# Kernel tuning notes

Hardware: AMD Instinct MI355X
Metric: run time of the kernel (lower is better)

The kernel has to match this reference:

```python
import jax, jax.numpy as jnp
import numpy as np

N_NODES = 100000
N_EDGES = 1600000
N_GRAPHS = 512
IN_DIM = 128
HID = 128
N_CLASSES = 10


def _gcn_conv(x, W, b, src, dst, n):
    """PyG GCNConv: out = D^{-1/2} (A+I) D^{-1/2} (x @ W) + b."""
    xw = x @ W  # [n, out_dim]
    loop = jnp.arange(n)
    s = jnp.concatenate([src, loop])  # add self loops
    d = jnp.concatenate([dst, loop])
    deg = jax.ops.segment_sum(jnp.ones(s.shape, dtype=xw.dtype), d, num_segments=n)
    dinv = jnp.where(deg > 0, jax.lax.rsqrt(deg), jnp.zeros((), xw.dtype))
    norm = dinv[s] * dinv[d]  # [E + n]
    out = jax.ops.segment_sum(xw[s] * norm[:, None], d, num_segments=n)
    return out + b


def _global_mean_pool(x, batch, num_graphs):
    sums = jax.ops.segment_sum(x, batch, num_segments=num_graphs)
    cnts = jax.ops.segment_sum(jnp.ones(batch.shape, dtype=x.dtype), batch, num_segments=num_graphs)
    return sums / jnp.maximum(cnts, 1.0)[:, None]


def setup_inputs() -> dict:
    key = jax.random.key(0)
    ks = jax.random.split(key, 8)
    x = jax.random.normal(ks[0], (N_NODES, IN_DIM), dtype=jnp.float32)
    edge_index = jax.random.randint(ks[1], (2, N_EDGES), 0, N_NODES, dtype=jnp.int64)
    batch = jnp.sort(jax.random.randint(ks[2], (N_NODES,), 0, N_GRAPHS, dtype=jnp.int64))
    sc = 1.0 / np.sqrt(IN_DIM)
    W1 = jax.random.normal(ks[3], (IN_DIM, HID), dtype=jnp.float32) * sc
    b1 = jnp.zeros((HID,), dtype=jnp.float32)
    W2 = jax.random.normal(ks[4], (HID, HID), dtype=jnp.float32) * (1.0 / np.sqrt(HID))
    b2 = jnp.zeros((HID,), dtype=jnp.float32)
    Wc = jax.random.normal(ks[5], (HID, N_CLASSES), dtype=jnp.float32) * (1.0 / np.sqrt(HID))
    bc = jnp.zeros((N_CLASSES,), dtype=jnp.float32)
    return {"x": x, "edge_index": edge_index, "batch": batch,
            "W1": W1, "b1": b1, "W2": W2, "b2": b2, "Wc": Wc, "bc": bc}


def reference(x, edge_index, batch, W1, b1, W2, b2, Wc, bc):
    src, dst = edge_index[0], edge_index[1]
    n = x.shape[0]
    h = _gcn_conv(x, W1, b1, src, dst, n)
    h = jax.nn.relu(h)
    h = _gcn_conv(h, W2, b2, src, dst, n)
    g = _global_mean_pool(h, batch, N_GRAPHS)
    return g @ Wc + bc
```

## Files before the change

kernel.cpp:

```cpp
#include <hip/hip_runtime.h>

#define N_NODES 100000
#define N_EDGES 1600000
#define N_GRAPHS 512
#define DIM 128
#define NCLS 10
#define NBKT 782
#define BCAP 2560

typedef __attribute__((ext_vector_type(8))) short short8;
typedef __attribute__((ext_vector_type(4))) float f32x4;

static __device__ __forceinline__ unsigned short f2bf(float f) {
    unsigned u = __float_as_uint(f);
    unsigned r = (u + 0x7FFF + ((u >> 16) & 1)) >> 16;
    return (unsigned short)r;
}
static __device__ __forceinline__ float bf2f(unsigned u) {
    return __uint_as_float(u << 16);
}


__global__ __launch_bounds__(256) void k_bucket(
    const int* __restrict__ src, const int* __restrict__ dst,
    int* __restrict__ bcnt, unsigned* __restrict__ bpack, int E) {
    __shared__ int cnt[NBKT];
    __shared__ int base[NBKT];
    int tid = threadIdx.x;
    for (int i = tid; i < NBKT; i += 256) cnt[i] = 0;
    __syncthreads();
    int e0 = blockIdx.x * 4096 + tid;
    unsigned pk[16]; short bk[16];
#pragma unroll
    for (int j = 0; j < 16; j++) {
        int e = e0 + j * 256;
        if (e < E) {
            int s = src[e], d = dst[e];
            bk[j] = (short)(d >> 7);
            pk[j] = ((unsigned)(d & 127) << 17) | (unsigned)s;
            atomicAdd(&cnt[bk[j]], 1);
        } else bk[j] = -1;
    }
    __syncthreads();
    for (int i = tid; i < NBKT; i += 256) {
        int c = cnt[i];
        base[i] = c ? atomicAdd(&bcnt[i], c) : 0;
        cnt[i] = 0;
    }
    __syncthreads();
#pragma unroll
    for (int j = 0; j < 16; j++) {
        if (bk[j] >= 0) {
            int p = base[bk[j]] + atomicAdd(&cnt[bk[j]], 1);
            if (p < BCAP) bpack[(size_t)bk[j] * BCAP + p] = pk[j];
        }
    }
}

__global__ __launch_bounds__(256) void k_bscan(const int* __restrict__ bcnt,
                                               int* __restrict__ bbase) {
    __shared__ int lds[256];
    int tid = threadIdx.x;
    int v[4], pre[4];
    int s = 0;
#pragma unroll
    for (int j = 0; j < 4; j++) {
        int idx = tid * 4 + j;
        v[j] = (idx < NBKT) ? min(bcnt[idx], BCAP) : 0;
        pre[j] = s; s += v[j];
    }
    lds[tid] = s;
    __syncthreads();
    for (int off = 1; off < 256; off <<= 1) {
        int t = (tid >= off) ? lds[tid - off] : 0;
        __syncthreads();
        lds[tid] += t;
        __syncthreads();
    }
    int excl = lds[tid] - s;
#pragma unroll
    for (int j = 0; j < 4; j++) {
        int idx = tid * 4 + j;
        if (idx < NBKT) bbase[idx] = excl + pre[j];
    }
}

__global__ __launch_bounds__(256) void k_bsort(
    const unsigned* __restrict__ bpack, const int* __restrict__ bcnt,
    const int* __restrict__ bbase, int* __restrict__ rp, float* __restrict__ dinv,
    int* __restrict__ esrc, int N) {
    __shared__ int cnt[128];
    __shared__ int scan[128];
    __shared__ int cur[128];
    int b = blockIdx.x, tid = threadIdx.x;
    int n0 = b << 7;
    int m = min(bcnt[b], BCAP);
    int gbase = bbase[b];
    const unsigned* bp = bpack + (size_t)b * BCAP;
    if (tid < 128) cnt[tid] = 0;
    __syncthreads();
    for (int j = tid; j < m; j += 256) atomicAdd(&cnt[bp[j] >> 17], 1);
    __syncthreads();
    if (tid < 128) scan[tid] = cnt[tid];
    __syncthreads();
    for (int off = 1; off < 128; off <<= 1) {
        int t = (tid < 128 && tid >= off) ? scan[tid - off] : 0;
        __syncthreads();
        if (tid < 128) scan[tid] += t;
        __syncthreads();
    }
    if (tid < 128) {
        int c = cnt[tid];
        int excl = scan[tid] - c;
        int node = n0 + tid;
        if (node <= N) rp[node] = gbase + excl;
        if (node < N) dinv[node] = rsqrtf((float)(c + 1));
        cur[tid] = gbase + excl;
    }
    __syncthreads();
    for (int j = tid; j < m; j += 256) {
        unsigned pk = bp[j];
        int p = atomicAdd(&cur[pk >> 17], 1);
        esrc[p] = (int)(pk & 0x1FFFF);
    }
}


__global__ void k_wprep(const float* __restrict__ W1, const float* __restrict__ W2,
                        unsigned short* __restrict__ wf1, unsigned short* __restrict__ wf2) {
    int b = blockIdx.x;
    const float* W = (b < 64) ? W1 : W2;
    unsigned short* wfrag = (b < 64) ? wf1 : wf2;
    int t = (b & 63) * 256 + threadIdx.x;
    int j = t & 7, lane = (t >> 3) & 63, nt = (t >> 9) & 7, kit = t >> 12;
    int k = kit * 32 + (lane >> 4) * 8 + j;
    int n = nt * 16 + (lane & 15);
    float v = W[k * 128 + n];
    unsigned short h = f2bf(v);
    wfrag[t] = h;
    wfrag[16384 + t] = f2bf(v - bf2f(h));
}


__global__ __launch_bounds__(256) void k_gemm_f32(
    const float* __restrict__ A, const unsigned short* __restrict__ wfrag,
    const float* __restrict__ dinv, unsigned short* __restrict__ ybf, int M) {
    __shared__ unsigned short scr[4 * 32 * 136];
    int tid = threadIdx.x, wave = tid >> 6, lane = tid & 63;
    int m = lane & 15, quad = lane >> 4;
    int rowBase = blockIdx.x * 128 + wave * 32;
    int r0 = rowBase + m, r1 = rowBase + 16 + m;
    f32x4 acc0[8], acc1[8];
#pragma unroll
    for (int i = 0; i < 8; i++) { acc0[i] = (f32x4){0,0,0,0}; acc1[i] = (f32x4){0,0,0,0}; }
    const unsigned short* whi = wfrag;
    const unsigned short* wlo = wfrag + 16384;

#pragma unroll
    for (int kit = 0; kit < 4; kit++) {
        float a0[8], a1[8];
        if (r0 < M) {
            const float4* ap = (const float4*)(A + (size_t)r0 * 128 + kit * 32 + quad * 8);
            float4 f0 = ap[0], f1 = ap[1];
            a0[0]=f0.x; a0[1]=f0.y; a0[2]=f0.z; a0[3]=f0.w; a0[4]=f1.x; a0[5]=f1.y; a0[6]=f1.z; a0[7]=f1.w;
        } else { for (int j = 0; j < 8; j++) a0[j] = 0.f; }
        if (r1 < M) {
            const float4* ap = (const float4*)(A + (size_t)r1 * 128 + kit * 32 + quad * 8);
            float4 f0 = ap[0], f1 = ap[1];
            a1[0]=f0.x; a1[1]=f0.y; a1[2]=f0.z; a1[3]=f0.w; a1[4]=f1.x; a1[5]=f1.y; a1[6]=f1.z; a1[7]=f1.w;
        } else { for (int j = 0; j < 8; j++) a1[j] = 0.f; }
        short8 ahi0, alo0, ahi1, alo1;
#pragma unroll
        for (int j = 0; j < 8; j++) {
            unsigned short h0 = f2bf(a0[j]);
            ahi0[j] = (short)h0; alo0[j] = (short)f2bf(a0[j] - bf2f(h0));
            unsigned short h1 = f2bf(a1[j]);
            ahi1[j] = (short)h1; alo1[j] = (short)f2bf(a1[j] - bf2f(h1));
        }
        int fb = kit * 4096 + lane * 8;
#pragma unroll
        for (int nt = 0; nt < 8; nt++) {
            int idx = fb + nt * 512;
            short8 bhi = *(const short8*)(whi + idx);
            short8 blo = *(const short8*)(wlo + idx);
            acc0[nt] = __builtin_amdgcn_mfma_f32_16x16x32_bf16(ahi0, bhi, acc0[nt], 0, 0, 0);
            acc0[nt] = __builtin_amdgcn_mfma_f32_16x16x32_bf16(alo0, bhi, acc0[nt], 0, 0, 0);
            acc0[nt] = __builtin_amdgcn_mfma_f32_16x16x32_bf16(ahi0, blo, acc0[nt], 0, 0, 0);
            acc1[nt] = __builtin_amdgcn_mfma_f32_16x16x32_bf16(ahi1, bhi, acc1[nt], 0, 0, 0);
            acc1[nt] = __builtin_amdgcn_mfma_f32_16x16x32_bf16(alo1, bhi, acc1[nt], 0, 0, 0);
            acc1[nt] = __builtin_amdgcn_mfma_f32_16x16x32_bf16(ahi1, blo, acc1[nt], 0, 0, 0);
        }
    }
    float dv0 = (r0 < M) ? dinv[r0] : 0.f;
    float dv1 = (r1 < M) ? dinv[r1] : 0.f;
    unsigned short* wsm = scr + wave * 32 * 136;
#pragma unroll
    for (int rg = 0; rg < 4; rg++) {
        float s0 = __shfl(dv0, quad * 4 + rg);
        float s1 = __shfl(dv1, quad * 4 + rg);
#pragma unroll
        for (int nt = 0; nt < 8; nt++) {
            wsm[(quad * 4 + rg) * 136 + nt * 16 + m] = f2bf(acc0[nt][rg] * s0);
            wsm[(16 + quad * 4 + rg) * 136 + nt * 16 + m] = f2bf(acc1[nt][rg] * s1);
        }
    }
    __syncthreads();
#pragma unroll
    for (int i = 0; i < 8; i++) {
        int rl = i * 4 + quad;
        int grow = rowBase + rl;
        if (grow < M) {
            short8 v = *(const short8*)(wsm + rl * 136 + m * 8);
            *(short8*)(ybf + (size_t)grow * 128 + m * 8) = v;
        }
    }
}


__global__ __launch_bounds__(256) void k_gemm_bf(
    const unsigned short* __restrict__ A, const unsigned short* __restrict__ wfrag,
    const float* __restrict__ dinv, unsigned short* __restrict__ ybf, int M) {
    __shared__ unsigned short scr[4 * 32 * 136];
    int tid = threadIdx.x, wave = tid >> 6, lane = tid & 63;
    int m = lane & 15, quad = lane >> 4;
    int rowBase = blockIdx.x * 128 + wave * 32;
    int r0 = rowBase + m, r1 = rowBase + 16 + m;
    f32x4 acc0[8], acc1[8];
#pragma unroll
    for (int i = 0; i < 8; i++) { acc0[i] = (f32x4){0,0,0,0}; acc1[i] = (f32x4){0,0,0,0}; }
    const unsigned short* whi = wfrag;
    const unsigned short* wlo = wfrag + 16384;

#pragma unroll
    for (int kit = 0; kit < 4; kit++) {
        short8 ah0, ah1;
        if (r0 < M) ah0 = *(const short8*)(A + (size_t)r0 * 128 + kit * 32 + quad * 8);
        else { for (int j = 0; j < 8; j++) ah0[j] = 0; }
        if (r1 < M) ah1 = *(const short8*)(A + (size_t)r1 * 128 + kit * 32 + quad * 8);
        else { for (int j = 0; j < 8; j++) ah1[j] = 0; }
        int fb = kit * 4096 + lane * 8;
#pragma unroll
        for (int nt = 0; nt < 8; nt++) {
            int idx = fb + nt * 512;
            short8 bhi = *(const short8*)(whi + idx);
            short8 blo = *(const short8*)(wlo + idx);
            acc0[nt] = __builtin_amdgcn_mfma_f32_16x16x32_bf16(ah0, bhi, acc0[nt], 0, 0, 0);
            acc0[nt] = __builtin_amdgcn_mfma_f32_16x16x32_bf16(ah0, blo, acc0[nt], 0, 0, 0);
            acc1[nt] = __builtin_amdgcn_mfma_f32_16x16x32_bf16(ah1, bhi, acc1[nt], 0, 0, 0);
            acc1[nt] = __builtin_amdgcn_mfma_f32_16x16x32_bf16(ah1, blo, acc1[nt], 0, 0, 0);
        }
    }
    float dv0 = (r0 < M) ? dinv[r0] : 0.f;
    float dv1 = (r1 < M) ? dinv[r1] : 0.f;
    unsigned short* wsm = scr + wave * 32 * 136;
#pragma unroll
    for (int rg = 0; rg < 4; rg++) {
        float s0 = __shfl(dv0, quad * 4 + rg);
        float s1 = __shfl(dv1, quad * 4 + rg);
#pragma unroll
        for (int nt = 0; nt < 8; nt++) {
            wsm[(quad * 4 + rg) * 136 + nt * 16 + m] = f2bf(acc0[nt][rg] * s0);
            wsm[(16 + quad * 4 + rg) * 136 + nt * 16 + m] = f2bf(acc1[nt][rg] * s1);
        }
    }
    __syncthreads();
#pragma unroll
    for (int i = 0; i < 8; i++) {
        int rl = i * 4 + quad;
        int grow = rowBase + rl;
        if (grow < M) {
            short8 v = *(const short8*)(wsm + rl * 136 + m * 8);
            *(short8*)(ybf + (size_t)grow * 128 + m * 8) = v;
        }
    }
}


__global__ __launch_bounds__(256) void k_agg(
    const unsigned short* __restrict__ y, const float* __restrict__ dinv,
    const int* __restrict__ rp, const int* __restrict__ esrc,
    const float* __restrict__ bias, unsigned* __restrict__ out, int relu, int N) {
    int wave = threadIdx.x >> 6;
    int lane = threadIdx.x & 63;
    int node = blockIdx.x * 4 + wave;
    if (node >= N) return;
    const unsigned* y2 = (const unsigned*)y;
    unsigned vs = y2[(size_t)node * 64 + lane];
    float a0 = bf2f(vs & 0xFFFF), a1 = bf2f(vs >> 16);
    int beg = rp[node], end = rp[node + 1];
    int j = beg;
    for (; j + 8 <= end; j += 8) {
        int s0 = esrc[j], s1 = esrc[j + 1], s2 = esrc[j + 2], s3 = esrc[j + 3];
        int s4 = esrc[j + 4], s5 = esrc[j + 5], s6 = esrc[j + 6], s7 = esrc[j + 7];
        unsigned v0 = y2[(size_t)s0 * 64 + lane];
        unsigned v1 = y2[(size_t)s1 * 64 + lane];
        unsigned v2 = y2[(size_t)s2 * 64 + lane];
        unsigned v3 = y2[(size_t)s3 * 64 + lane];
        unsigned v4 = y2[(size_t)s4 * 64 + lane];
        unsigned v5 = y2[(size_t)s5 * 64 + lane];
        unsigned v6 = y2[(size_t)s6 * 64 + lane];
        unsigned v7 = y2[(size_t)s7 * 64 + lane];
        a0 += bf2f(v0 & 0xFFFF); a1 += bf2f(v0 >> 16);
        a0 += bf2f(v1 & 0xFFFF); a1 += bf2f(v1 >> 16);
        a0 += bf2f(v2 & 0xFFFF); a1 += bf2f(v2 >> 16);
        a0 += bf2f(v3 & 0xFFFF); a1 += bf2f(v3 >> 16);
        a0 += bf2f(v4 & 0xFFFF); a1 += bf2f(v4 >> 16);
        a0 += bf2f(v5 & 0xFFFF); a1 += bf2f(v5 >> 16);
        a0 += bf2f(v6 & 0xFFFF); a1 += bf2f(v6 >> 16);
        a0 += bf2f(v7 & 0xFFFF); a1 += bf2f(v7 >> 16);
    }
    for (; j < end; j++) {
        unsigned v = y2[(size_t)esrc[j] * 64 + lane];
        a0 += bf2f(v & 0xFFFF); a1 += bf2f(v >> 16);
    }
    float s = dinv[node];
    float2 bv = ((const float2*)bias)[lane];
    float o0 = s * a0 + bv.x;
    float o1 = s * a1 + bv.y;
    if (relu) { o0 = fmaxf(o0, 0.f); o1 = fmaxf(o1, 0.f); }
    out[(size_t)node * 64 + lane] = (unsigned)f2bf(o0) | ((unsigned)f2bf(o1) << 16);
}


__global__ __launch_bounds__(256) void k_poolhead(
    const unsigned* __restrict__ h2, const int* __restrict__ batch,
    const float* __restrict__ Wc, const float* __restrict__ bc,
    float* __restrict__ out, int n) {
    __shared__ float2 red[4][64];
    __shared__ float grow[DIM];
    int gid = blockIdx.x;
    int tid = threadIdx.x, wave = tid >> 6, lane = tid & 63;
    int lo = 0, hi = n;
    while (lo < hi) { int mid = (lo + hi) >> 1; if (batch[mid] < gid) lo = mid + 1; else hi = mid; }
    int start = lo;
    hi = n;
    while (lo < hi) { int mid = (lo + hi) >> 1; if (batch[mid] < gid + 1) lo = mid + 1; else hi = mid; }
    int end = lo;
    float a0 = 0.f, a1 = 0.f;
    for (int r = start + wave; r < end; r += 4) {
        unsigned v = h2[(size_t)r * 64 + lane];
        a0 += bf2f(v & 0xFFFF); a1 += bf2f(v >> 16);
    }
    red[wave][lane] = make_float2(a0, a1);
    __syncthreads();
    if (tid < 64) {
        float2 s = red[0][tid];
        s.x += red[1][tid].x; s.y += red[1][tid].y;
        s.x += red[2][tid].x; s.y += red[2][tid].y;
        s.x += red[3][tid].x; s.y += red[3][tid].y;
        int cnt = end - start;
        float inv = 1.f / (float)(cnt > 0 ? cnt : 1);
        grow[tid * 2] = s.x * inv;
        grow[tid * 2 + 1] = s.y * inv;
    }
    __syncthreads();
    if (tid < NCLS) {
        float acc = bc[tid];
#pragma unroll 16
        for (int k = 0; k < DIM; k++) acc += grow[k] * Wc[k * NCLS + tid];
        out[gid * NCLS + tid] = acc;
    }
}

extern "C" void kernel_launch(void* const* d_in, const int* in_sizes, int n_in,
                              void* d_out, int out_size, void* d_ws, size_t ws_size,
                              hipStream_t stream) {
    const float* x    = (const float*)d_in[0];
    const int*   ei   = (const int*)d_in[1];
    const int*   batch= (const int*)d_in[2];
    const float* W1   = (const float*)d_in[3];
    const float* b1   = (const float*)d_in[4];
    const float* W2   = (const float*)d_in[5];
    const float* b2   = (const float*)d_in[6];
    const float* Wc   = (const float*)d_in[7];
    const float* bc   = (const float*)d_in[8];
    float* out = (float*)d_out;
    const int N = N_NODES, E = N_EDGES;
    const int* src = ei;
    const int* dst = ei + E;

    char* ws = (char*)d_ws;
    size_t off = 0;
    auto carve = [&](size_t bytes) -> void* {
        void* p = ws + off;
        off = (off + bytes + 255) & ~(size_t)255;
        return p;
    };
    int*      rp    = (int*)     carve((size_t)(N + 1) * 4);
    float*    dinv  = (float*)   carve((size_t)N * 4);
    int*      bcnt  = (int*)     carve(NBKT * 4);
    int*      bbase = (int*)     carve(NBKT * 4);
    unsigned* bpack = (unsigned*)carve((size_t)NBKT * BCAP * 4);
    int*      esrc  = (int*)     carve((size_t)E * 4);
    unsigned short* wf1 = (unsigned short*)carve(2 * 16384 * 2);
    unsigned short* wf2 = (unsigned short*)carve(2 * 16384 * 2);
    unsigned short* bufY = (unsigned short*)carve((size_t)N * DIM * 2);
    unsigned short* bufH = (unsigned short*)carve((size_t)N * DIM * 2);
    (void)ws_size; (void)n_in; (void)in_sizes; (void)out_size;

    hipMemsetAsync(bcnt, 0, NBKT * 4, stream);
    hipLaunchKernelGGL(k_wprep,  dim3(128), dim3(256), 0, stream, W1, W2, wf1, wf2);
    hipLaunchKernelGGL(k_bucket, dim3((E + 4095) / 4096), dim3(256), 0, stream, src, dst, bcnt, bpack, E);
    hipLaunchKernelGGL(k_bscan,  dim3(1), dim3(256), 0, stream, bcnt, bbase);
    hipLaunchKernelGGL(k_bsort,  dim3(NBKT), dim3(256), 0, stream, bpack, bcnt, bbase, rp, dinv, esrc, N);

    int gemmGrid = (N + 127) / 128;
    hipLaunchKernelGGL(k_gemm_f32, dim3(gemmGrid), dim3(256), 0, stream, x, wf1, dinv, bufY, N);
    hipLaunchKernelGGL(k_agg, dim3((N + 3) / 4), dim3(256), 0, stream, bufY, dinv, rp, esrc, b1, (unsigned*)bufH, 1, N);
    hipLaunchKernelGGL(k_gemm_bf, dim3(gemmGrid), dim3(256), 0, stream, bufH, wf2, dinv, bufY, N);
    hipLaunchKernelGGL(k_agg, dim3((N + 3) / 4), dim3(256), 0, stream, bufY, dinv, rp, esrc, b2, (unsigned*)bufH, 0, N);
    hipLaunchKernelGGL(k_poolhead, dim3(N_GRAPHS), dim3(256), 0, stream, (const unsigned*)bufH, batch, Wc, bc, out, N);
}
```

Measured before the change: 375.3 us.

## Fold memset and bucket scan into other kernels, stage weights in LDS, wave-load edge indices

Zeroing the bucket counters moves into extra blocks of the weight-prep kernel, which drops the memset. The single-block bucket scan is now recomputed redundantly inside every bucket-sort block, which removes two launches. Both GEMM kernels copy the high-part weight fragments into shared memory and read them from there. The aggregation loop loads up to 64 edge indices per wave in one coalesced load and broadcasts them with shuffles instead of issuing scalar index loads.

```diff
diff --git a/kernel.cpp b/kernel.cpp
--- a/kernel.cpp
+++ b/kernel.cpp
@@ -21,114 +21,15 @@
 }
 
 
-__global__ __launch_bounds__(256) void k_bucket(
-    const int* __restrict__ src, const int* __restrict__ dst,
-    int* __restrict__ bcnt, unsigned* __restrict__ bpack, int E) {
-    __shared__ int cnt[NBKT];
-    __shared__ int base[NBKT];
-    int tid = threadIdx.x;
-    for (int i = tid; i < NBKT; i += 256) cnt[i] = 0;
-    __syncthreads();
-    int e0 = blockIdx.x * 4096 + tid;
-    unsigned pk[16]; short bk[16];
-#pragma unroll
-    for (int j = 0; j < 16; j++) {
-        int e = e0 + j * 256;
-        if (e < E) {
-            int s = src[e], d = dst[e];
-            bk[j] = (short)(d >> 7);
-            pk[j] = ((unsigned)(d & 127) << 17) | (unsigned)s;
-            atomicAdd(&cnt[bk[j]], 1);
-        } else bk[j] = -1;
-    }
-    __syncthreads();
-    for (int i = tid; i < NBKT; i += 256) {
-        int c = cnt[i];
-        base[i] = c ? atomicAdd(&bcnt[i], c) : 0;
-        cnt[i] = 0;
-    }
-    __syncthreads();
-#pragma unroll
-    for (int j = 0; j < 16; j++) {
-        if (bk[j] >= 0) {
-            int p = base[bk[j]] + atomicAdd(&cnt[bk[j]], 1);
-            if (p < BCAP) bpack[(size_t)bk[j] * BCAP + p] = pk[j];
-        }
-    }
-}
-
-__global__ __launch_bounds__(256) void k_bscan(const int* __restrict__ bcnt,
-                                               int* __restrict__ bbase) {
-    __shared__ int lds[256];
-    int tid = threadIdx.x;
-    int v[4], pre[4];
-    int s = 0;
-#pragma unroll
-    for (int j = 0; j < 4; j++) {
-        int idx = tid * 4 + j;
-        v[j] = (idx < NBKT) ? min(bcnt[idx], BCAP) : 0;
-        pre[j] = s; s += v[j];
-    }
-    lds[tid] = s;
-    __syncthreads();
-    for (int off = 1; off < 256; off <<= 1) {
-        int t = (tid >= off) ? lds[tid - off] : 0;
-        __syncthreads();
-        lds[tid] += t;
-        __syncthreads();
-    }
-    int excl = lds[tid] - s;
-#pragma unroll
-    for (int j = 0; j < 4; j++) {
-        int idx = tid * 4 + j;
-        if (idx < NBKT) bbase[idx] = excl + pre[j];
-    }
-}
-
-__global__ __launch_bounds__(256) void k_bsort(
-    const unsigned* __restrict__ bpack, const int* __restrict__ bcnt,
-    const int* __restrict__ bbase, int* __restrict__ rp, float* __restrict__ dinv,
-    int* __restrict__ esrc, int N) {
-    __shared__ int cnt[128];
-    __shared__ int scan[128];
-    __shared__ int cur[128];
-    int b = blockIdx.x, tid = threadIdx.x;
-    int n0 = b << 7;
-    int m = min(bcnt[b], BCAP);
-    int gbase = bbase[b];
-    const unsigned* bp = bpack + (size_t)b * BCAP;
-    if (tid < 128) cnt[tid] = 0;
-    __syncthreads();
-    for (int j = tid; j < m; j += 256) atomicAdd(&cnt[bp[j] >> 17], 1);
-    __syncthreads();
-    if (tid < 128) scan[tid] = cnt[tid];
-    __syncthreads();
-    for (int off = 1; off < 128; off <<= 1) {
-        int t = (tid < 128 && tid >= off) ? scan[tid - off] : 0;
-        __syncthreads();
-        if (tid < 128) scan[tid] += t;
-        __syncthreads();
-    }
-    if (tid < 128) {
-        int c = cnt[tid];
-        int excl = scan[tid] - c;
-        int node = n0 + tid;
-        if (node <= N) rp[node] = gbase + excl;
-        if (node < N) dinv[node] = rsqrtf((float)(c + 1));
-        cur[tid] = gbase + excl;
-    }
-    __syncthreads();
-    for (int j = tid; j < m; j += 256) {
-        unsigned pk = bp[j];
-        int p = atomicAdd(&cur[pk >> 17], 1);
-        esrc[p] = (int)(pk & 0x1FFFF);
-    }
-}
-
-
 __global__ void k_wprep(const float* __restrict__ W1, const float* __restrict__ W2,
-                        unsigned short* __restrict__ wf1, unsigned short* __restrict__ wf2) {
+                        unsigned short* __restrict__ wf1, unsigned short* __restrict__ wf2,
+                        int* __restrict__ bcnt) {
     int b = blockIdx.x;
+    if (b >= 128) {
+        int i = (b - 128) * 256 + threadIdx.x;
+        if (i < NBKT) bcnt[i] = 0;
+        return;
+    }
     const float* W = (b < 64) ? W1 : W2;
     unsigned short* wfrag = (b < 64) ? wf1 : wf2;
     int t = (b & 63) * 256 + threadIdx.x;
@@ -142,18 +43,117 @@
 }
 
 
+__global__ __launch_bounds__(256) void k_bucket(
+    const int* __restrict__ src, const int* __restrict__ dst,
+    int* __restrict__ bcnt, unsigned* __restrict__ bpack, int E) {
+    __shared__ int cnt[NBKT];
+    __shared__ int base[NBKT];
+    int tid = threadIdx.x;
+    for (int i = tid; i < NBKT; i += 256) cnt[i] = 0;
+    __syncthreads();
+    int e0 = blockIdx.x * 4096 + tid;
+    unsigned pk[16]; short bk[16];
+#pragma unroll
+    for (int j = 0; j < 16; j++) {
+        int e = e0 + j * 256;
+        if (e < E) {
+            int s = src[e], d = dst[e];
+            bk[j] = (short)(d >> 7);
+            pk[j] = ((unsigned)(d & 127) << 17) | (unsigned)s;
+            atomicAdd(&cnt[bk[j]], 1);
+        } else bk[j] = -1;
+    }
+    __syncthreads();
+    for (int i = tid; i < NBKT; i += 256) {
+        int c = cnt[i];
+        base[i] = c ? atomicAdd(&bcnt[i], c) : 0;
+        cnt[i] = 0;
+    }
+    __syncthreads();
+#pragma unroll
+    for (int j = 0; j < 16; j++) {
+        if (bk[j] >= 0) {
+            int p = base[bk[j]] + atomicAdd(&cnt[bk[j]], 1);
+            if (p < BCAP) bpack[(size_t)bk[j] * BCAP + p] = pk[j];
+        }
+    }
+}
+
+
+__global__ __launch_bounds__(256) void k_bsort(
+    const unsigned* __restrict__ bpack, const int* __restrict__ bcnt,
+    int* __restrict__ rp, float* __restrict__ dinv,
+    int* __restrict__ esrc, int N) {
+    __shared__ int lds[256];
+    __shared__ int gbase_sh;
+    __shared__ int cnt[128];
+    __shared__ int scan[128];
+    __shared__ int cur[128];
+    int b = blockIdx.x, tid = threadIdx.x;
+    int v[4], pre[4];
+    int s = 0;
+#pragma unroll
+    for (int j = 0; j < 4; j++) {
+        int idx = tid * 4 + j;
+        v[j] = (idx < NBKT) ? min(bcnt[idx], BCAP) : 0;
+        pre[j] = s; s += v[j];
+    }
+    lds[tid] = s;
+    __syncthreads();
+    for (int off = 1; off < 256; off <<= 1) {
+        int t = (tid >= off) ? lds[tid - off] : 0;
+        __syncthreads();
+        lds[tid] += t;
+        __syncthreads();
+    }
+    if (tid == (b >> 2)) gbase_sh = lds[tid] - s + pre[b & 3];
+    if (tid < 128) cnt[tid] = 0;
+    __syncthreads();
+    int gbase = gbase_sh;
+    int n0 = b << 7;
+    int m = min(bcnt[b], BCAP);
+    const unsigned* bp = bpack + (size_t)b * BCAP;
+    for (int j = tid; j < m; j += 256) atomicAdd(&cnt[bp[j] >> 17], 1);
+    __syncthreads();
+    if (tid < 128) scan[tid] = cnt[tid];
+    __syncthreads();
+    for (int off = 1; off < 128; off <<= 1) {
+        int t = (tid < 128 && tid >= off) ? scan[tid - off] : 0;
+        __syncthreads();
+        if (tid < 128) scan[tid] += t;
+        __syncthreads();
+    }
+    if (tid < 128) {
+        int c = cnt[tid];
+        int excl = scan[tid] - c;
+        int node = n0 + tid;
+        if (node <= N) rp[node] = gbase + excl;
+        if (node < N) dinv[node] = rsqrtf((float)(c + 1));
+        cur[tid] = gbase + excl;
+    }
+    __syncthreads();
+    for (int j = tid; j < m; j += 256) {
+        unsigned pk = bp[j];
+        int p = atomicAdd(&cur[pk >> 17], 1);
+        esrc[p] = (int)(pk & 0x1FFFF);
+    }
+}
+
+
 __global__ __launch_bounds__(256) void k_gemm_f32(
     const float* __restrict__ A, const unsigned short* __restrict__ wfrag,
     const float* __restrict__ dinv, unsigned short* __restrict__ ybf, int M) {
-    __shared__ unsigned short scr[4 * 32 * 136];
+    __shared__ unsigned short ldsw[4 * 32 * 136];
     int tid = threadIdx.x, wave = tid >> 6, lane = tid & 63;
     int m = lane & 15, quad = lane >> 4;
     int rowBase = blockIdx.x * 128 + wave * 32;
     int r0 = rowBase + m, r1 = rowBase + 16 + m;
+    for (int i = tid; i < 2048; i += 256)
+        ((short8*)ldsw)[i] = ((const short8*)wfrag)[i];
+    __syncthreads();
     f32x4 acc0[8], acc1[8];
 #pragma unroll
     for (int i = 0; i < 8; i++) { acc0[i] = (f32x4){0,0,0,0}; acc1[i] = (f32x4){0,0,0,0}; }
-    const unsigned short* whi = wfrag;
     const unsigned short* wlo = wfrag + 16384;
 
 #pragma unroll
@@ -181,7 +181,7 @@
 #pragma unroll
         for (int nt = 0; nt < 8; nt++) {
             int idx = fb + nt * 512;
-            short8 bhi = *(const short8*)(whi + idx);
+            short8 bhi = *(const short8*)(ldsw + idx);
             short8 blo = *(const short8*)(wlo + idx);
             acc0[nt] = __builtin_amdgcn_mfma_f32_16x16x32_bf16(ahi0, bhi, acc0[nt], 0, 0, 0);
             acc0[nt] = __builtin_amdgcn_mfma_f32_16x16x32_bf16(alo0, bhi, acc0[nt], 0, 0, 0);
@@ -191,9 +191,10 @@
             acc1[nt] = __builtin_amdgcn_mfma_f32_16x16x32_bf16(ahi1, blo, acc1[nt], 0, 0, 0);
         }
     }
+    __syncthreads();
     float dv0 = (r0 < M) ? dinv[r0] : 0.f;
     float dv1 = (r1 < M) ? dinv[r1] : 0.f;
-    unsigned short* wsm = scr + wave * 32 * 136;
+    unsigned short* wsm = ldsw + wave * 32 * 136;
 #pragma unroll
     for (int rg = 0; rg < 4; rg++) {
         float s0 = __shfl(dv0, quad * 4 + rg);
@@ -220,15 +221,17 @@
 __global__ __launch_bounds__(256) void k_gemm_bf(
     const unsigned short* __restrict__ A, const unsigned short* __restrict__ wfrag,
     const float* __restrict__ dinv, unsigned short* __restrict__ ybf, int M) {
-    __shared__ unsigned short scr[4 * 32 * 136];
+    __shared__ unsigned short ldsw[4 * 32 * 136];
     int tid = threadIdx.x, wave = tid >> 6, lane = tid & 63;
     int m = lane & 15, quad = lane >> 4;
     int rowBase = blockIdx.x * 128 + wave * 32;
     int r0 = rowBase + m, r1 = rowBase + 16 + m;
+    for (int i = tid; i < 2048; i += 256)
+        ((short8*)ldsw)[i] = ((const short8*)wfrag)[i];
+    __syncthreads();
     f32x4 acc0[8], acc1[8];
 #pragma unroll
     for (int i = 0; i < 8; i++) { acc0[i] = (f32x4){0,0,0,0}; acc1[i] = (f32x4){0,0,0,0}; }
-    const unsigned short* whi = wfrag;
     const unsigned short* wlo = wfrag + 16384;
 
 #pragma unroll
@@ -242,7 +245,7 @@
 #pragma unroll
         for (int nt = 0; nt < 8; nt++) {
             int idx = fb + nt * 512;
-            short8 bhi = *(const short8*)(whi + idx);
+            short8 bhi = *(const short8*)(ldsw + idx);
             short8 blo = *(const short8*)(wlo + idx);
             acc0[nt] = __builtin_amdgcn_mfma_f32_16x16x32_bf16(ah0, bhi, acc0[nt], 0, 0, 0);
             acc0[nt] = __builtin_amdgcn_mfma_f32_16x16x32_bf16(ah0, blo, acc0[nt], 0, 0, 0);
@@ -250,9 +253,10 @@
             acc1[nt] = __builtin_amdgcn_mfma_f32_16x16x32_bf16(ah1, blo, acc1[nt], 0, 0, 0);
         }
     }
+    __syncthreads();
     float dv0 = (r0 < M) ? dinv[r0] : 0.f;
     float dv1 = (r1 < M) ? dinv[r1] : 0.f;
-    unsigned short* wsm = scr + wave * 32 * 136;
+    unsigned short* wsm = ldsw + wave * 32 * 136;
 #pragma unroll
     for (int rg = 0; rg < 4; rg++) {
         float s0 = __shfl(dv0, quad * 4 + rg);
@@ -289,29 +293,30 @@
     float a0 = bf2f(vs & 0xFFFF), a1 = bf2f(vs >> 16);
     int beg = rp[node], end = rp[node + 1];
     int j = beg;
-    for (; j + 8 <= end; j += 8) {
-        int s0 = esrc[j], s1 = esrc[j + 1], s2 = esrc[j + 2], s3 = esrc[j + 3];
-        int s4 = esrc[j + 4], s5 = esrc[j + 5], s6 = esrc[j + 6], s7 = esrc[j + 7];
-        unsigned v0 = y2[(size_t)s0 * 64 + lane];
-        unsigned v1 = y2[(size_t)s1 * 64 + lane];
-        unsigned v2 = y2[(size_t)s2 * 64 + lane];
-        unsigned v3 = y2[(size_t)s3 * 64 + lane];
-        unsigned v4 = y2[(size_t)s4 * 64 + lane];
-        unsigned v5 = y2[(size_t)s5 * 64 + lane];
-        unsigned v6 = y2[(size_t)s6 * 64 + lane];
-        unsigned v7 = y2[(size_t)s7 * 64 + lane];
-        a0 += bf2f(v0 & 0xFFFF); a1 += bf2f(v0 >> 16);
-        a0 += bf2f(v1 & 0xFFFF); a1 += bf2f(v1 >> 16);
-        a0 += bf2f(v2 & 0xFFFF); a1 += bf2f(v2 >> 16);
-        a0 += bf2f(v3 & 0xFFFF); a1 += bf2f(v3 >> 16);
-        a0 += bf2f(v4 & 0xFFFF); a1 += bf2f(v4 >> 16);
-        a0 += bf2f(v5 & 0xFFFF); a1 += bf2f(v5 >> 16);
-        a0 += bf2f(v6 & 0xFFFF); a1 += bf2f(v6 >> 16);
-        a0 += bf2f(v7 & 0xFFFF); a1 += bf2f(v7 >> 16);
-    }
-    for (; j < end; j++) {
-        unsigned v = y2[(size_t)esrc[j] * 64 + lane];
-        a0 += bf2f(v & 0xFFFF); a1 += bf2f(v >> 16);
+    while (j < end) {
+        int idxv = (j + lane < end) ? esrc[j + lane] : 0;
+        int cnt = end - j; if (cnt > 64) cnt = 64;
+        int i = 0;
+        for (; i + 4 <= cnt; i += 4) {
+            int s0 = __shfl(idxv, i + 0);
+            int s1 = __shfl(idxv, i + 1);
+            int s2 = __shfl(idxv, i + 2);
+            int s3 = __shfl(idxv, i + 3);
+            unsigned v0 = y2[(size_t)s0 * 64 + lane];
+            unsigned v1 = y2[(size_t)s1 * 64 + lane];
+            unsigned v2 = y2[(size_t)s2 * 64 + lane];
+            unsigned v3 = y2[(size_t)s3 * 64 + lane];
+            a0 += bf2f(v0 & 0xFFFF); a1 += bf2f(v0 >> 16);
+            a0 += bf2f(v1 & 0xFFFF); a1 += bf2f(v1 >> 16);
+            a0 += bf2f(v2 & 0xFFFF); a1 += bf2f(v2 >> 16);
+            a0 += bf2f(v3 & 0xFFFF); a1 += bf2f(v3 >> 16);
+        }
+        for (; i < cnt; i++) {
+            int s = __shfl(idxv, i);
+            unsigned v = y2[(size_t)s * 64 + lane];
+            a0 += bf2f(v & 0xFFFF); a1 += bf2f(v >> 16);
+        }
+        j += cnt;
     }
     float s = dinv[node];
     float2 bv = ((const float2*)bias)[lane];
@@ -389,7 +394,6 @@
     int*      rp    = (int*)     carve((size_t)(N + 1) * 4);
     float*    dinv  = (float*)   carve((size_t)N * 4);
     int*      bcnt  = (int*)     carve(NBKT * 4);
-    int*      bbase = (int*)     carve(NBKT * 4);
     unsigned* bpack = (unsigned*)carve((size_t)NBKT * BCAP * 4);
     int*      esrc  = (int*)     carve((size_t)E * 4);
     unsigned short* wf1 = (unsigned short*)carve(2 * 16384 * 2);
@@ -398,11 +402,9 @@
     unsigned short* bufH = (unsigned short*)carve((size_t)N * DIM * 2);
     (void)ws_size; (void)n_in; (void)in_sizes; (void)out_size;
 
-    hipMemsetAsync(bcnt, 0, NBKT * 4, stream);
-    hipLaunchKernelGGL(k_wprep,  dim3(128), dim3(256), 0, stream, W1, W2, wf1, wf2);
+    hipLaunchKernelGGL(k_wprep,  dim3(128 + (NBKT + 255) / 256), dim3(256), 0, stream, W1, W2, wf1, wf2, bcnt);
     hipLaunchKernelGGL(k_bucket, dim3((E + 4095) / 4096), dim3(256), 0, stream, src, dst, bcnt, bpack, E);
-    hipLaunchKernelGGL(k_bscan,  dim3(1), dim3(256), 0, stream, bcnt, bbase);
-    hipLaunchKernelGGL(k_bsort,  dim3(NBKT), dim3(256), 0, stream, bpack, bcnt, bbase, rp, dinv, esrc, N);
+    hipLaunchKernelGGL(k_bsort,  dim3(NBKT), dim3(256), 0, stream, bpack, bcnt, rp, dinv, esrc, N);
 
     int gemmGrid = (N + 127) / 128;
     hipLaunchKernelGGL(k_gemm_f32, dim3(gemmGrid), dim3(256), 0, stream, x, wf1, dinv, bufY, N);
```

After: 343.3 us (median of 2 runs). 8.5% less time.
